# Optimization experiments

Measured on AMD Instinct MI355X. Metric: run time of the kernel, lower is better.

Reference implementation:

```python
import jax, jax.numpy as jnp
import numpy as np

EMBED = 1024
HEADS = 16
HEAD_DIM = EMBED // HEADS


def setup_inputs() -> dict:
    key = jax.random.key(0)
    ks = jax.random.split(key, 8)
    N, S = 4, 2048
    scale = 0.02
    return {
        "query": jax.random.normal(ks[0], (N, S, EMBED), jnp.float32),
        "keys": jax.random.normal(ks[1], (N, S, EMBED), jnp.float32),
        "values": jax.random.normal(ks[2], (N, S, EMBED), jnp.float32),
        "Wq": jax.random.normal(ks[3], (HEAD_DIM, HEAD_DIM), jnp.float32) * scale,
        "Wk": jax.random.normal(ks[4], (HEAD_DIM, HEAD_DIM), jnp.float32) * scale,
        "Wv": jax.random.normal(ks[5], (HEAD_DIM, HEAD_DIM), jnp.float32) * scale,
        "Wo": jax.random.normal(ks[6], (EMBED, EMBED), jnp.float32) * scale,
        "bo": jax.random.normal(ks[7], (EMBED,), jnp.float32) * scale,
    }


def reference(query, keys, values, Wq, Wk, Wv, Wo, bo):
    N, Q, _ = query.shape
    K = keys.shape[1]
    # split heads: [N, len, H, D]
    q = query.reshape(N, Q, HEADS, HEAD_DIM)
    k = keys.reshape(N, K, HEADS, HEAD_DIM)
    v = values.reshape(N, K, HEADS, HEAD_DIM)
    # per-head linear projections (torch Linear: x @ W.T), shared across heads
    q = jnp.einsum('nqhd,ed->nqhe', q, Wq)
    k = jnp.einsum('nkhd,ed->nkhe', k, Wk)
    v = jnp.einsum('nkhd,ed->nkhe', v, Wv)
    # attention scores [N, H, Q, K]; note: scaled by sqrt(embed_size), as in source
    energy = jnp.einsum('nqhd,nkhd->nhqk', q, k)
    attn = jax.nn.softmax(energy / jnp.sqrt(jnp.float32(EMBED)), axis=-1)
    out = jnp.einsum('nhqk,nkhd->nqhd', attn, v).reshape(N, Q, EMBED)
    return out @ Wo.T + bo
```

## Files before the change

kernel.cpp:

```cpp
#include <hip/hip_runtime.h>

#define EMBED 1024
#define HEADS 16
#define HDIM 64
#define SEQ 2048
#define NBATCH 4
#define KVSTRIDE 136

typedef __bf16 bf16;
typedef __bf16 b8v __attribute__((ext_vector_type(8)));
typedef __bf16 b4v __attribute__((ext_vector_type(4)));
typedef float f4v __attribute__((ext_vector_type(4)));
typedef float f16v __attribute__((ext_vector_type(16)));
typedef unsigned long long u64;

#define QSCALE 0.045084220027780106f

static __device__ __forceinline__ f16v mfma32(b8v a, b8v b, f16v c) {
  return __builtin_amdgcn_mfma_f32_32x32x16_bf16(a, b, c, 0, 0, 0);
}

static __device__ __forceinline__ b8v lds_b8(const char* p) {
  const b4v lo = *reinterpret_cast<const b4v*>(p);
  const b4v h4 = *reinterpret_cast<const b4v*>(p + 8);
  b8v r;
#pragma unroll
  for (int j = 0; j < 4; ++j) { r[j] = lo[j]; r[4 + j] = h4[j]; }
  return r;
}

__global__ __launch_bounds__(256) void proj_kernel(
    const float* __restrict__ q_in, const float* __restrict__ k_in,
    const float* __restrict__ v_in, const float* __restrict__ Wq,
    const float* __restrict__ Wk, const float* __restrict__ Wv,
    const float* __restrict__ Wo, bf16* __restrict__ Qp,
    bf16* __restrict__ Kp, bf16* __restrict__ VpT, bf16* __restrict__ Wb) {
  const int mode = blockIdx.y;
  const int tid = threadIdx.x;

  if (mode == 3) {
    const int i = (blockIdx.x * 256 + tid) * 4;
    const f4v v = *reinterpret_cast<const f4v*>(Wo + i);
    b4v o;
    o[0] = (bf16)v[0]; o[1] = (bf16)v[1]; o[2] = (bf16)v[2]; o[3] = (bf16)v[3];
    *reinterpret_cast<b4v*>(Wb + i) = o;
    return;
  }

  __shared__ __align__(16) char xl[128 * KVSTRIDE];
  __shared__ __align__(16) char wl[64 * KVSTRIDE];
  __shared__ __align__(16) char ol[128 * KVSTRIDE];

  const float* x = (mode == 0) ? q_in : (mode == 1) ? k_in : v_in;
  const float* W = (mode == 0) ? Wq : (mode == 1) ? Wk : Wv;
  const float wscale = (mode == 0) ? QSCALE : 1.0f;

  const int lane = tid & 63, wave = tid >> 6;
  const int l31 = lane & 31, hi = lane >> 5;
  const int bid = blockIdx.x;
  const int stile = bid & 15, nh = bid >> 4;
  const int n = nh >> 4, h = nh & 15;
  const int s0 = stile * 128;

  const float* xb = x + (size_t)(n * SEQ + s0) * EMBED + h * HDIM;
#pragma unroll
  for (int r = 0; r < 8; ++r) {
    const int idx = r * 256 + tid;
    const int row = idx >> 4, c = idx & 15;
    const f4v v = *reinterpret_cast<const f4v*>(xb + (size_t)row * EMBED + c * 4);
    b4v o;
    o[0] = (bf16)v[0]; o[1] = (bf16)v[1]; o[2] = (bf16)v[2]; o[3] = (bf16)v[3];
    *reinterpret_cast<b4v*>(xl + row * KVSTRIDE + c * 8) = o;
  }
#pragma unroll
  for (int r = 0; r < 4; ++r) {
    const int idx = r * 256 + tid;
    const int row = idx >> 4, c = idx & 15;
    const f4v v = *reinterpret_cast<const f4v*>(W + row * 64 + c * 4);
    b4v o;
    o[0] = (bf16)(v[0] * wscale); o[1] = (bf16)(v[1] * wscale);
    o[2] = (bf16)(v[2] * wscale); o[3] = (bf16)(v[3] * wscale);
    *reinterpret_cast<b4v*>(wl + row * KVSTRIDE + c * 8) = o;
  }
  __syncthreads();

  const int s0w = wave * 32;
  b8v wf[2][4], xf[4];
#pragma unroll
  for (int eb = 0; eb < 2; ++eb)
#pragma unroll
    for (int dk = 0; dk < 4; ++dk)
      wf[eb][dk] = lds_b8(wl + (eb * 32 + l31) * KVSTRIDE + dk * 32 + hi * 16);
#pragma unroll
  for (int dk = 0; dk < 4; ++dk)
    xf[dk] = lds_b8(xl + (s0w + l31) * KVSTRIDE + dk * 32 + hi * 16);

  if (mode < 2) {
#pragma unroll
    for (int eb = 0; eb < 2; ++eb) {
      f16v d;
#pragma unroll
      for (int i = 0; i < 16; ++i) d[i] = 0.f;
#pragma unroll
      for (int dk = 0; dk < 4; ++dk) d = mfma32(wf[eb][dk], xf[dk], d);
      char* orow = ol + (s0w + l31) * KVSTRIDE + eb * 64 + hi * 8;
#pragma unroll
      for (int qd = 0; qd < 4; ++qd) {
        b4v o;
#pragma unroll
        for (int rr = 0; rr < 4; ++rr) o[rr] = (bf16)d[qd * 4 + rr];
        *reinterpret_cast<b4v*>(orow + qd * 16) = o;
      }
    }
  } else {
#pragma unroll
    for (int eb = 0; eb < 2; ++eb) {
      f16v d;
#pragma unroll
      for (int i = 0; i < 16; ++i) d[i] = 0.f;
#pragma unroll
      for (int dk = 0; dk < 4; ++dk) d = mfma32(xf[dk], wf[eb][dk], d);
      char* orow = ol + (eb * 32 + l31) * 264 + s0w * 2 + hi * 8;
#pragma unroll
      for (int qd = 0; qd < 4; ++qd) {
        b4v o;
#pragma unroll
        for (int rr = 0; rr < 4; ++rr) o[rr] = (bf16)d[qd * 4 + rr];
        *reinterpret_cast<b4v*>(orow + qd * 16) = o;
      }
    }
  }
  __syncthreads();

  if (mode < 2) {
    bf16* outb = ((mode == 0) ? Qp : Kp) + (size_t)nh * SEQ * HDIM +
                 (size_t)s0 * HDIM;
#pragma unroll
    for (int r = 0; r < 4; ++r) {
      const int idx = r * 256 + tid;
      const int row = idx >> 3, c8 = idx & 7;
      const u64 a = *reinterpret_cast<const u64*>(ol + row * KVSTRIDE + c8 * 16);
      const u64 b = *reinterpret_cast<const u64*>(ol + row * KVSTRIDE + c8 * 16 + 8);
      uint4 v;
      v.x = (unsigned)a; v.y = (unsigned)(a >> 32);
      v.z = (unsigned)b; v.w = (unsigned)(b >> 32);
      *reinterpret_cast<uint4*>(outb + (size_t)row * HDIM + c8 * 8) = v;
    }
  } else {
    bf16* outb = VpT + (size_t)nh * HDIM * SEQ + s0;
#pragma unroll
    for (int r = 0; r < 4; ++r) {
      const int idx = r * 256 + tid;
      const int row = idx >> 4, c = idx & 15;
      const u64 a = *reinterpret_cast<const u64*>(ol + row * 264 + c * 16);
      const u64 b = *reinterpret_cast<const u64*>(ol + row * 264 + c * 16 + 8);
      uint4 v;
      v.x = (unsigned)a; v.y = (unsigned)(a >> 32);
      v.z = (unsigned)b; v.w = (unsigned)(b >> 32);
      *reinterpret_cast<uint4*>(outb + (size_t)row * SEQ + c * 8) = v;
    }
  }
}

__global__ __launch_bounds__(256, 2) void attn_kernel(
    const bf16* __restrict__ Qp, const bf16* __restrict__ Kp,
    const bf16* __restrict__ VpT, bf16* __restrict__ O) {
  __shared__ __align__(16) char smem[2][2][64 * KVSTRIDE];

  const int tid = threadIdx.x;
  const int lane = tid & 63, wave = tid >> 6;
  const int l31 = lane & 31, hi = lane >> 5;

  const int bid = blockIdx.x;
  const int nh = bid & 63, qb = bid >> 6;
  const int n = nh >> 4, h = nh & 15;
  const int q0 = qb * 256 + wave * 64;

  const bf16* Qnh = Qp + (size_t)nh * SEQ * HDIM;
  const bf16* Knh = Kp + (size_t)nh * SEQ * HDIM;
  const bf16* Vnh = VpT + (size_t)nh * HDIM * SEQ;

  b8v bq[2][4];
#pragma unroll
  for (int qt = 0; qt < 2; ++qt)
#pragma unroll
    for (int dk = 0; dk < 4; ++dk)
      bq[qt][dk] = *reinterpret_cast<const b8v*>(
          Qnh + (size_t)(q0 + qt * 32 + l31) * HDIM + dk * 16 + hi * 8);

  f16v acc[2][2];
#pragma unroll
  for (int qt = 0; qt < 2; ++qt)
#pragma unroll
    for (int dblk = 0; dblk < 2; ++dblk)
#pragma unroll
      for (int i = 0; i < 16; ++i) acc[qt][dblk][i] = 0.f;
  float lsum0 = 0.f, lsum1 = 0.f;

  const int srow = tid >> 3, seg = tid & 7;
  uint4 kst[2], vst[2];

#define G_ISSUE(kv0)                                                           \
  {                                                                            \
    kst[0] = *reinterpret_cast<const uint4*>(Knh + (size_t)((kv0) + srow) * HDIM + seg * 8); \
    kst[1] = *reinterpret_cast<const uint4*>(Knh + (size_t)((kv0) + srow + 32) * HDIM + seg * 8); \
    vst[0] = *reinterpret_cast<const uint4*>(Vnh + (size_t)srow * SEQ + (kv0) + seg * 8); \
    vst[1] = *reinterpret_cast<const uint4*>(Vnh + (size_t)(srow + 32) * SEQ + (kv0) + seg * 8); \
  }

#define L_WRITE(c)                                                             \
  {                                                                            \
    _Pragma("unroll")                                                          \
    for (int rr = 0; rr < 2; ++rr) {                                           \
      char* kd = &smem[c][0][(srow + 32 * rr) * KVSTRIDE + seg * 16];          \
      const u64* kp = reinterpret_cast<const u64*>(&kst[rr]);                  \
      *reinterpret_cast<u64*>(kd) = kp[0];                                     \
      *reinterpret_cast<u64*>(kd + 8) = kp[1];                                 \
      char* vd = &smem[c][1][(srow + 32 * rr) * KVSTRIDE + seg * 16];          \
      const u64* vp = reinterpret_cast<const u64*>(&vst[rr]);                  \
      *reinterpret_cast<u64*>(vd) = vp[0];                                     \
      *reinterpret_cast<u64*>(vd + 8) = vp[1];                                 \
    }                                                                          \
  }

  G_ISSUE(0);
  L_WRITE(0);
  __syncthreads();
  int cur = 0;

  for (int t = 0; t < SEQ / 64; ++t) {
    if (t + 1 < SEQ / 64) G_ISSUE((t + 1) * 64);

    const char* kb = smem[cur][0];
    const char* vb = smem[cur][1];

    b8v pa[2][2][2];
    float ps0 = 0.f, ps1 = 0.f;
#pragma unroll
    for (int g = 0; g < 2; ++g) {
      f16v sA, sB;
#pragma unroll
      for (int i = 0; i < 16; ++i) { sA[i] = 0.f; sB[i] = 0.f; }
      const char* kr = kb + (g * 32 + l31) * KVSTRIDE + hi * 16;
      __builtin_amdgcn_s_setprio(1);
#pragma unroll
      for (int dk = 0; dk < 4; ++dk) {
        const b4v klo = *reinterpret_cast<const b4v*>(kr + dk * 32);
        const b4v khi = *reinterpret_cast<const b4v*>(kr + dk * 32 + 8);
        b8v ak;
#pragma unroll
        for (int j = 0; j < 4; ++j) { ak[j] = klo[j]; ak[4 + j] = khi[j]; }
        sA = mfma32(ak, bq[0][dk], sA);
        sB = mfma32(ak, bq[1][dk], sB);
      }
      __builtin_amdgcn_s_setprio(0);
#pragma unroll
      for (int reg = 0; reg < 16; ++reg) {
        const float p = __builtin_amdgcn_exp2f(sA[reg]);
        ps0 += p;
        pa[0][g][reg >> 3][reg & 7] = (bf16)p;
      }
#pragma unroll
      for (int reg = 0; reg < 16; ++reg) {
        const float p = __builtin_amdgcn_exp2f(sB[reg]);
        ps1 += p;
        pa[1][g][reg >> 3][reg & 7] = (bf16)p;
      }
    }
    ps0 += __shfl_xor(ps0, 32);
    ps1 += __shfl_xor(ps1, 32);
    lsum0 += ps0;
    lsum1 += ps1;

    __builtin_amdgcn_s_setprio(1);
#pragma unroll
    for (int dblk = 0; dblk < 2; ++dblk) {
      const char* vr = vb + (dblk * 32 + l31) * KVSTRIDE + hi * 8;
#pragma unroll
      for (int g = 0; g < 2; ++g)
#pragma unroll
        for (int kc = 0; kc < 2; ++kc) {
          const b4v lo = *reinterpret_cast<const b4v*>(vr + g * 64 + kc * 32);
          const b4v h4 = *reinterpret_cast<const b4v*>(vr + g * 64 + kc * 32 + 16);
          b8v bv;
#pragma unroll
          for (int j = 0; j < 4; ++j) { bv[j] = lo[j]; bv[4 + j] = h4[j]; }
          acc[0][dblk] = mfma32(pa[0][g][kc], bv, acc[0][dblk]);
          acc[1][dblk] = mfma32(pa[1][g][kc], bv, acc[1][dblk]);
        }
    }
    __builtin_amdgcn_s_setprio(0);

    if (t + 1 < SEQ / 64) L_WRITE(cur ^ 1);
    __syncthreads();
    cur ^= 1;
  }

#pragma unroll
  for (int qt = 0; qt < 2; ++qt) {
    const float ls = (qt == 0) ? lsum0 : lsum1;
#pragma unroll
    for (int reg = 0; reg < 16; ++reg) {
      const int qrow = (reg & 3) + 8 * (reg >> 2) + 4 * hi;
      const float rinv = __builtin_amdgcn_rcpf(__shfl(ls, qrow, 64));
#pragma unroll
      for (int dblk = 0; dblk < 2; ++dblk) {
        O[(size_t)(n * SEQ + q0 + qt * 32 + qrow) * EMBED + h * HDIM +
          dblk * 32 + l31] = (bf16)(acc[qt][dblk][reg] * rinv);
      }
    }
  }
#undef G_ISSUE
#undef L_WRITE
}

__global__ __launch_bounds__(256) void out_gemm(
    const bf16* __restrict__ O, const bf16* __restrict__ Wb,
    const float* __restrict__ bo, float* __restrict__ Y) {
  __shared__ __align__(16) char smem[2][2][128 * KVSTRIDE];

  const int tid = threadIdx.x;
  const int lane = tid & 63, wave = tid >> 6;
  const int l31 = lane & 31, hi = lane >> 5;
  const int m0 = blockIdx.x * 128;
  const int j0 = blockIdx.y * 128;
  const int mw = (wave >> 1) * 64, jw = (wave & 1) * 64;

  f16v acc[2][2];
#pragma unroll
  for (int mt = 0; mt < 2; ++mt)
#pragma unroll
    for (int jt = 0; jt < 2; ++jt)
#pragma unroll
      for (int i = 0; i < 16; ++i) acc[mt][jt][i] = 0.f;

  const bf16* Ab = O + (size_t)m0 * EMBED;
  const bf16* Bb = Wb + (size_t)j0 * EMBED;
  const int srow = tid >> 3, seg = tid & 7;
  uint4 ast[4], bst[4];

#define G_ISSUE(kt)                                                            \
  {                                                                            \
    _Pragma("unroll")                                                          \
    for (int rr = 0; rr < 4; ++rr) {                                           \
      ast[rr] = *reinterpret_cast<const uint4*>(                               \
          Ab + (size_t)(srow + 32 * rr) * EMBED + (kt) * 64 + seg * 8);        \
      bst[rr] = *reinterpret_cast<const uint4*>(                               \
          Bb + (size_t)(srow + 32 * rr) * EMBED + (kt) * 64 + seg * 8);        \
    }                                                                          \
  }

#define L_WRITE(c)                                                             \
  {                                                                            \
    _Pragma("unroll")                                                          \
    for (int rr = 0; rr < 4; ++rr) {                                           \
      char* ad = &smem[c][0][(srow + 32 * rr) * KVSTRIDE + seg * 16];          \
      const u64* ap = reinterpret_cast<const u64*>(&ast[rr]);                  \
      *reinterpret_cast<u64*>(ad) = ap[0];                                     \
      *reinterpret_cast<u64*>(ad + 8) = ap[1];                                 \
      char* bd = &smem[c][1][(srow + 32 * rr) * KVSTRIDE + seg * 16];          \
      const u64* bp = reinterpret_cast<const u64*>(&bst[rr]);                  \
      *reinterpret_cast<u64*>(bd) = bp[0];                                     \
      *reinterpret_cast<u64*>(bd + 8) = bp[1];                                 \
    }                                                                          \
  }

  G_ISSUE(0);
  L_WRITE(0);
  __syncthreads();
  int cur = 0;

  for (int kt = 0; kt < EMBED / 64; ++kt) {
    if (kt + 1 < EMBED / 64) G_ISSUE(kt + 1);

    const char* at = smem[cur][0];
    const char* bt = smem[cur][1];

    __builtin_amdgcn_s_setprio(1);
#pragma unroll
    for (int dk = 0; dk < 4; ++dk) {
      b8v a[2], b[2];
#pragma unroll
      for (int mt = 0; mt < 2; ++mt)
        a[mt] = lds_b8(at + (mw + mt * 32 + l31) * KVSTRIDE + dk * 32 + hi * 16);
#pragma unroll
      for (int jt = 0; jt < 2; ++jt)
        b[jt] = lds_b8(bt + (jw + jt * 32 + l31) * KVSTRIDE + dk * 32 + hi * 16);
      acc[0][0] = mfma32(a[0], b[0], acc[0][0]);
      acc[0][1] = mfma32(a[0], b[1], acc[0][1]);
      acc[1][0] = mfma32(a[1], b[0], acc[1][0]);
      acc[1][1] = mfma32(a[1], b[1], acc[1][1]);
    }
    __builtin_amdgcn_s_setprio(0);

    if (kt + 1 < EMBED / 64) L_WRITE(cur ^ 1);
    __syncthreads();
    cur ^= 1;
  }

#pragma unroll
  for (int jt = 0; jt < 2; ++jt) {
    const float bias = bo[j0 + jw + jt * 32 + l31];
#pragma unroll
    for (int mt = 0; mt < 2; ++mt)
#pragma unroll
      for (int reg = 0; reg < 16; ++reg) {
        const int mrow = (reg & 3) + 8 * (reg >> 2) + 4 * hi;
        Y[(size_t)(m0 + mw + mt * 32 + mrow) * EMBED + j0 + jw + jt * 32 + l31] =
            acc[mt][jt][reg] + bias;
      }
  }
#undef G_ISSUE
#undef L_WRITE
}

extern "C" void kernel_launch(void* const* d_in, const int* in_sizes, int n_in,
                              void* d_out, int out_size, void* d_ws, size_t ws_size,
                              hipStream_t stream) {
  const float* query  = (const float*)d_in[0];
  const float* keys   = (const float*)d_in[1];
  const float* values = (const float*)d_in[2];
  const float* Wq = (const float*)d_in[3];
  const float* Wk = (const float*)d_in[4];
  const float* Wv = (const float*)d_in[5];
  const float* Wo = (const float*)d_in[6];
  const float* bo = (const float*)d_in[7];
  float* Y = (float*)d_out;

  char* ws = (char*)d_ws;
  const size_t szP = (size_t)NBATCH * HEADS * SEQ * HDIM * sizeof(bf16);
  bf16* Qp  = (bf16*)(ws);
  bf16* Kp  = (bf16*)(ws + szP);
  bf16* VpT = (bf16*)(ws + 2 * szP);
  bf16* O   = (bf16*)(ws + 3 * szP);
  bf16* Wb  = (bf16*)(ws + 4 * szP);

  proj_kernel<<<dim3(1024, 4), dim3(256), 0, stream>>>(
      query, keys, values, Wq, Wk, Wv, Wo, Qp, Kp, VpT, Wb);
  attn_kernel<<<dim3(512), dim3(256), 0, stream>>>(Qp, Kp, VpT, O);
  out_gemm<<<dim3(64, 8), dim3(256), 0, stream>>>(O, Wb, bo, Y);
}
```

Measured before the change: 127.2 us.

## Software-pipeline attention loop with triple-buffered KV and interleaved QK/PV stages

```diff
diff --git a/kernel.cpp b/kernel.cpp
--- a/kernel.cpp
+++ b/kernel.cpp
@@ -6,6 +6,8 @@
 #define SEQ 2048
 #define NBATCH 4
 #define KVSTRIDE 136
+#define VOFF (64 * KVSTRIDE)
+#define NT (SEQ / 64)
 
 typedef __bf16 bf16;
 typedef __bf16 b8v __attribute__((ext_vector_type(8)));
@@ -165,7 +167,7 @@
 __global__ __launch_bounds__(256, 2) void attn_kernel(
     const bf16* __restrict__ Qp, const bf16* __restrict__ Kp,
     const bf16* __restrict__ VpT, bf16* __restrict__ O) {
-  __shared__ __align__(16) char smem[2][2][64 * KVSTRIDE];
+  __shared__ __align__(16) char smem[3][2 * 64 * KVSTRIDE];
 
   const int tid = threadIdx.x;
   const int lane = tid & 63, wave = tid >> 6;
@@ -208,93 +210,125 @@
     vst[1] = *reinterpret_cast<const uint4*>(Vnh + (size_t)(srow + 32) * SEQ + (kv0) + seg * 8); \
   }
 
-#define L_WRITE(c)                                                             \
+#define L_WRITE(base)                                                          \
   {                                                                            \
     _Pragma("unroll")                                                          \
     for (int rr = 0; rr < 2; ++rr) {                                           \
-      char* kd = &smem[c][0][(srow + 32 * rr) * KVSTRIDE + seg * 16];          \
+      char* kd = (base) + (srow + 32 * rr) * KVSTRIDE + seg * 16;              \
       const u64* kp = reinterpret_cast<const u64*>(&kst[rr]);                  \
       *reinterpret_cast<u64*>(kd) = kp[0];                                     \
       *reinterpret_cast<u64*>(kd + 8) = kp[1];                                 \
-      char* vd = &smem[c][1][(srow + 32 * rr) * KVSTRIDE + seg * 16];          \
+      char* vd = (base) + VOFF + (srow + 32 * rr) * KVSTRIDE + seg * 16;       \
       const u64* vp = reinterpret_cast<const u64*>(&vst[rr]);                  \
       *reinterpret_cast<u64*>(vd) = vp[0];                                     \
       *reinterpret_cast<u64*>(vd + 8) = vp[1];                                 \
     }                                                                          \
   }
 
+#define QK_TILE(kbase, s)                                                      \
+  {                                                                            \
+    _Pragma("unroll")                                                          \
+    for (int g = 0; g < 2; ++g) {                                              \
+      _Pragma("unroll")                                                        \
+      for (int i = 0; i < 16; ++i) { s[0][g][i] = 0.f; s[1][g][i] = 0.f; }     \
+      const char* kr = (kbase) + (g * 32 + l31) * KVSTRIDE + hi * 16;          \
+      _Pragma("unroll")                                                        \
+      for (int dk = 0; dk < 4; ++dk) {                                         \
+        const b8v ak = lds_b8(kr + dk * 32);                                   \
+        s[0][g] = mfma32(ak, bq[0][dk], s[0][g]);                              \
+        s[1][g] = mfma32(ak, bq[1][dk], s[1][g]);                              \
+      }                                                                        \
+    }                                                                          \
+  }
+
+#define EXP_QT(sg0, sg1, pa, psum)                                             \
+  {                                                                            \
+    _Pragma("unroll")                                                          \
+    for (int reg = 0; reg < 16; ++reg) {                                       \
+      const float p0 = __builtin_amdgcn_exp2f(sg0[reg]);                       \
+      const float p1 = __builtin_amdgcn_exp2f(sg1[reg]);                       \
+      psum += p0 + p1;                                                         \
+      pa[0][reg >> 3][reg & 7] = (bf16)p0;                                     \
+      pa[1][reg >> 3][reg & 7] = (bf16)p1;                                     \
+    }                                                                          \
+  }
+
+#define PV_DBLK(vbase, dblk, paA, paB)                                         \
+  {                                                                            \
+    const char* vr = (vbase) + VOFF + ((dblk) * 32 + l31) * KVSTRIDE + hi * 8; \
+    _Pragma("unroll")                                                          \
+    for (int g = 0; g < 2; ++g) {                                              \
+      _Pragma("unroll")                                                        \
+      for (int kc = 0; kc < 2; ++kc) {                                         \
+        const b4v lo = *reinterpret_cast<const b4v*>(vr + g * 64 + kc * 32);   \
+        const b4v h4 = *reinterpret_cast<const b4v*>(vr + g * 64 + kc * 32 + 16); \
+        b8v bv;                                                                \
+        _Pragma("unroll")                                                      \
+        for (int j = 0; j < 4; ++j) { bv[j] = lo[j]; bv[4 + j] = h4[j]; }      \
+        acc[0][dblk] = mfma32(paA[g][kc], bv, acc[0][dblk]);                   \
+        acc[1][dblk] = mfma32(paB[g][kc], bv, acc[1][dblk]);                   \
+      }                                                                        \
+    }                                                                          \
+  }
+
   G_ISSUE(0);
-  L_WRITE(0);
+  L_WRITE(smem[0]);
+  G_ISSUE(64);
+  L_WRITE(smem[1]);
   __syncthreads();
-  int cur = 0;
-
-  for (int t = 0; t < SEQ / 64; ++t) {
-    if (t + 1 < SEQ / 64) G_ISSUE((t + 1) * 64);
-
-    const char* kb = smem[cur][0];
-    const char* vb = smem[cur][1];
-
-    b8v pa[2][2][2];
+
+  char* pC = smem[0];
+  char* pN = smem[1];
+  char* pF = smem[2];
+
+  b8v paP[2][2][2];
+  {
+    f16v s[2][2];
+    QK_TILE(pC, s);
     float ps0 = 0.f, ps1 = 0.f;
-#pragma unroll
-    for (int g = 0; g < 2; ++g) {
-      f16v sA, sB;
-#pragma unroll
-      for (int i = 0; i < 16; ++i) { sA[i] = 0.f; sB[i] = 0.f; }
-      const char* kr = kb + (g * 32 + l31) * KVSTRIDE + hi * 16;
-      __builtin_amdgcn_s_setprio(1);
-#pragma unroll
-      for (int dk = 0; dk < 4; ++dk) {
-        const b4v klo = *reinterpret_cast<const b4v*>(kr + dk * 32);
-        const b4v khi = *reinterpret_cast<const b4v*>(kr + dk * 32 + 8);
-        b8v ak;
-#pragma unroll
-        for (int j = 0; j < 4; ++j) { ak[j] = klo[j]; ak[4 + j] = khi[j]; }
-        sA = mfma32(ak, bq[0][dk], sA);
-        sB = mfma32(ak, bq[1][dk], sB);
-      }
-      __builtin_amdgcn_s_setprio(0);
-#pragma unroll
-      for (int reg = 0; reg < 16; ++reg) {
-        const float p = __builtin_amdgcn_exp2f(sA[reg]);
-        ps0 += p;
-        pa[0][g][reg >> 3][reg & 7] = (bf16)p;
-      }
-#pragma unroll
-      for (int reg = 0; reg < 16; ++reg) {
-        const float p = __builtin_amdgcn_exp2f(sB[reg]);
-        ps1 += p;
-        pa[1][g][reg >> 3][reg & 7] = (bf16)p;
-      }
-    }
-    ps0 += __shfl_xor(ps0, 32);
-    ps1 += __shfl_xor(ps1, 32);
+    EXP_QT(s[0][0], s[0][1], paP[0], ps0);
+    EXP_QT(s[1][0], s[1][1], paP[1], ps1);
     lsum0 += ps0;
     lsum1 += ps1;
-
+  }
+
+  for (int t = 0; t < NT - 1; ++t) {
+    const bool more = (t + 2 < NT);
+    if (more) G_ISSUE((t + 2) * 64);
+
+    f16v s[2][2];
     __builtin_amdgcn_s_setprio(1);
-#pragma unroll
-    for (int dblk = 0; dblk < 2; ++dblk) {
-      const char* vr = vb + (dblk * 32 + l31) * KVSTRIDE + hi * 8;
+    QK_TILE(pN, s);
+    __builtin_amdgcn_s_setprio(0);
+
+    b8v paN[2][2][2];
+    float ps0 = 0.f, ps1 = 0.f;
+    PV_DBLK(pC, 0, paP[0], paP[1]);
+    EXP_QT(s[0][0], s[0][1], paN[0], ps0);
+    PV_DBLK(pC, 1, paP[0], paP[1]);
+    EXP_QT(s[1][0], s[1][1], paN[1], ps1);
+    lsum0 += ps0;
+    lsum1 += ps1;
+
+    if (more) L_WRITE(pF);
+
+#pragma unroll
+    for (int qt = 0; qt < 2; ++qt)
 #pragma unroll
       for (int g = 0; g < 2; ++g)
 #pragma unroll
-        for (int kc = 0; kc < 2; ++kc) {
-          const b4v lo = *reinterpret_cast<const b4v*>(vr + g * 64 + kc * 32);
-          const b4v h4 = *reinterpret_cast<const b4v*>(vr + g * 64 + kc * 32 + 16);
-          b8v bv;
-#pragma unroll
-          for (int j = 0; j < 4; ++j) { bv[j] = lo[j]; bv[4 + j] = h4[j]; }
-          acc[0][dblk] = mfma32(pa[0][g][kc], bv, acc[0][dblk]);
-          acc[1][dblk] = mfma32(pa[1][g][kc], bv, acc[1][dblk]);
-        }
-    }
-    __builtin_amdgcn_s_setprio(0);
-
-    if (t + 1 < SEQ / 64) L_WRITE(cur ^ 1);
+        for (int kc = 0; kc < 2; ++kc) paP[qt][g][kc] = paN[qt][g][kc];
+    char* tmp = pC; pC = pN; pN = pF; pF = tmp;
     __syncthreads();
-    cur ^= 1;
-  }
+  }
+
+  __builtin_amdgcn_s_setprio(1);
+  PV_DBLK(pC, 0, paP[0], paP[1]);
+  PV_DBLK(pC, 1, paP[0], paP[1]);
+  __builtin_amdgcn_s_setprio(0);
+
+  lsum0 += __shfl_xor(lsum0, 32);
+  lsum1 += __shfl_xor(lsum1, 32);
 
 #pragma unroll
   for (int qt = 0; qt < 2; ++qt) {
@@ -312,6 +346,9 @@
   }
 #undef G_ISSUE
 #undef L_WRITE
+#undef QK_TILE
+#undef EXP_QT
+#undef PV_DBLK
 }
 
 __global__ __launch_bounds__(256) void out_gemm(
```

Result: faster. 122.9 us (median of 2 runs) (-3.4%).
